# Kernel optimization log

Hardware: AMD Instinct MI355X
Metric: run time of the kernel (lower is better)

The kernel has to match this reference:

```python
import jax, jax.numpy as jnp
import numpy as np

FC = 16  # feat_channel
EPS = 1e-4


def _sch_forward(sch_feat, conv_weight, mask, target, pre_ind, ind):
    B, C, H, W = sch_feat.shape
    M = pre_ind.shape[1]
    fc = FC
    # _tranpose_and_gather_feat: gather per-object weight vectors at pre_ind
    cw = conv_weight.reshape(B, conv_weight.shape[1], H * W)          # B,Wt,HW
    weight = jnp.take_along_axis(cw, pre_ind[:, None, :], axis=2)    # B,Wt,M
    weight = jnp.transpose(weight, (0, 2, 1))                         # B,M,Wt
    # split into the 3-layer dynamic MLP params
    s1 = (fc + 2) * fc
    w1 = weight[..., :s1].reshape(B, M, fc, fc + 2)
    b1 = weight[..., s1:s1 + fc]
    s2 = s1 + fc
    w2 = weight[..., s2:s2 + fc * fc].reshape(B, M, fc, fc)
    b2 = weight[..., s2 + fc * fc:s2 + fc * fc + fc]
    s3 = s2 + fc * fc + fc
    w3 = weight[..., s3:s3 + fc]                                      # B,M,fc (1 out channel)
    b3 = weight[..., s3 + fc:s3 + fc + 1]                             # B,M,1
    # relative coordinate grids; note torch: x = pre_ind % w (int), y = pre_ind / w (true div)
    x = (pre_ind % W).astype(jnp.float32)
    y = pre_ind.astype(jnp.float32) / W
    xg = jnp.arange(W, dtype=jnp.float32)
    yg = jnp.arange(H, dtype=jnp.float32)
    x_rel = (xg[None, None, None, :] - x[:, :, None, None]) / 128.0   # B,M,1,W
    y_rel = (yg[None, None, :, None] - y[:, :, None, None]) / 128.0   # B,M,H,1
    x_rel = jnp.broadcast_to(x_rel, (B, M, H, W))
    y_rel = jnp.broadcast_to(y_rel, (B, M, H, W))
    feat = jnp.concatenate([
        jnp.broadcast_to(sch_feat[:, None], (B, M, C, H, W)),
        x_rel[:, :, None], y_rel[:, :, None]], axis=2)                # B,M,fc+2,H,W
    # three grouped 1x1 convs == per-instance matmuls
    h = jax.nn.relu(jnp.einsum('bmchw,bmoc->bmohw', feat, w1) + b1[:, :, :, None, None])
    h = jax.nn.relu(jnp.einsum('bmchw,bmoc->bmohw', h, w2) + b2[:, :, :, None, None])
    hm = jnp.einsum('bmchw,bmc->bmhw', h, w3) + b3[:, :, :, None]      # B,M,H,W
    hm = jnp.clip(jax.nn.sigmoid(hm), EPS, 1.0 - EPS)                  # _sigmoid
    # FastFocalLoss over (B*M, 1, H, W) with cat = 0
    neg_loss = jnp.sum(jnp.log(1.0 - hm) * hm ** 2 * (1.0 - target) ** 4)
    hm_flat = hm.reshape(B, M, H * W)
    pos_pred = jnp.take_along_axis(hm_flat, ind[..., None], axis=2)[..., 0]  # B,M
    pos_loss = jnp.sum(jnp.log(pos_pred) * (1.0 - pos_pred) ** 2 * mask)
    num_pos = jnp.sum(mask)
    loss = jnp.where(num_pos == 0,
                     -neg_loss,
                     -(pos_loss + neg_loss) / jnp.maximum(num_pos, 1.0))
    return loss


def setup_inputs() -> dict:
    key = jax.random.key(0)
    k1, k2, k3, k4, k5 = jax.random.split(key, 5)
    B, M, H, W = 4, 32, 152, 272
    Wt = (FC + 2) * FC + FC + FC * FC + FC + FC + 1  # 593
    return {
        'sch_feat': jax.random.normal(k1, (B, FC, H, W), dtype=jnp.float32),
        'conv_weight': jax.random.normal(k2, (B, Wt, H, W), dtype=jnp.float32),
        'mask': jnp.ones((B, M), dtype=jnp.float32),
        'pre_ind': jax.random.randint(k3, (B, M), 0, H * W, dtype=jnp.int64) if jax.config.jax_enable_x64 else jax.random.randint(k3, (B, M), 0, H * W).astype(jnp.int32),
        'target': jax.random.uniform(k4, (B, M, H, W), dtype=jnp.float32),
        'ind': jax.random.randint(k5, (B, M), 0, H * W).astype(jnp.int32),
    }


def reference(sch_feat, conv_weight, mask, pre_ind, target, ind):
    return _sch_forward(sch_feat, conv_weight, mask, target, pre_ind, ind)
```

## Files before the change

### kernel.cpp

```cpp
#include <hip/hip_runtime.h>

typedef unsigned int uint;
typedef unsigned short ushort;

constexpr int Bc = 4, Mc = 32, Hc = 152, Wc = 272;
constexpr int HWc = Hc * Wc;
constexpr int WTc = 593;
constexpr int MG = 4;
constexpr int MPB = 8;
constexpr int NBCH = 64;
constexpr int NEG_BLOCKS = Bc * MG * NBCH;
constexpr int ITERS = HWc / 64;
constexpr int POS_OFF = 1024;
constexpr int APK1_OFF = 2048;
constexpr int APK2_OFF = APK1_OFF + 128 * 64 * 4;
constexpr int W3B3_OFF = APK2_OFF + 128 * 64 * 4;
constexpr int CB_OFF   = W3B3_OFF + 128 * 20;
constexpr size_t XOFF_BYTES = (size_t)(CB_OFF + 128 * 32) * 4;
constexpr int GRPB = HWc / 16;
constexpr int GSTRIDE = 576;
constexpr int XCVT_BLOCKS = 162 * Bc;

using f32x4 = __attribute__((ext_vector_type(4))) float;
using bf16x8 = __attribute__((ext_vector_type(8))) short;

__device__ inline uint pkbf(float lo, float hi) {
  uint r;
  asm("v_cvt_pk_bf16_f32 %0, %1, %2" : "=v"(r) : "v"(lo), "v"(hi));
  return r;
}

__device__ inline float xsum16(float x) {
#if __has_builtin(__builtin_amdgcn_permlane16_swap)
  uint u = __float_as_uint(x);
  auto pr = __builtin_amdgcn_permlane16_swap(u, u, false, false);
  return __uint_as_float(pr[0]) + __uint_as_float(pr[1]);
#else
  return x + __shfl_xor(x, 16);
#endif
}
__device__ inline float xsum32(float x) {
#if __has_builtin(__builtin_amdgcn_permlane32_swap)
  uint u = __float_as_uint(x);
  auto pr = __builtin_amdgcn_permlane32_swap(u, u, false, false);
  return __uint_as_float(pr[0]) + __uint_as_float(pr[1]);
#else
  return x + __shfl_xor(x, 32);
#endif
}

union FR { uint u[4]; bf16x8 v; };

__global__ __launch_bounds__(256) void fused_pre(const float* __restrict__ sf_all,
                                                 const float* __restrict__ cw,
                                                 const int* __restrict__ pre_ind,
                                                 const int* __restrict__ ind,
                                                 const float* __restrict__ mask,
                                                 unsigned char* __restrict__ xb,
                                                 float* __restrict__ ws) {
  __shared__ float sw[WTc];
  __shared__ float sh1[16], sh2[16];
  const int blk = blockIdx.x, tid = threadIdx.x;

  if (blk < XCVT_BLOCKS) {
    const int b = blk / 162, bx = blk - b * 162;
    const int px = bx * 256 + tid;
    if (px < HWc) {
      const float* s = sf_all + (size_t)b * 16 * HWc + px;
      uint q[8];
#pragma unroll
      for (int i = 0; i < 8; i++) q[i] = pkbf(s[(size_t)(2 * i) * HWc], s[(size_t)(2 * i + 1) * HWc]);
      const int hh = px / Wc, xx = px - hh * Wc;
      const uint q8 = pkbf((float)xx * 0.0078125f, (float)hh * 0.0078125f);
      const int grp = px >> 4, o = px & 15;
      unsigned char* gb = xb + ((size_t)b * GRPB + grp) * GSTRIDE;
      *(uint4*)(gb + o * 16) = make_uint4(q[0], q[1], q[2], q[3]);
      *(uint4*)(gb + 256 + o * 16) = make_uint4(q[4], q[5], q[6], q[7]);
      *(uint*)(gb + 512 + o * 4) = q8;
    }
    return;
  }

  const int bm = blk - XCVT_BLOCKS, b = bm >> 5;
  const int p = pre_ind[bm];
  const float* wcol = cw + (size_t)b * WTc * HWc + p;
  for (int j = tid; j < WTc; j += 256) sw[j] = wcol[(size_t)j * HWc];
  __syncthreads();

  const float x0 = (float)(p % Wc);
  const float y0 = (float)p / (float)Wc;

  if (tid < 64) {
    const int g = tid >> 4, o = tid & 15;
    float a1f[8], a2f[8];
#pragma unroll
    for (int e = 0; e < 8; e++) {
      int k = 8 * g + e;
      a1f[e] = (k < 18) ? sw[o * 18 + k] : 0.0f;
      a2f[e] = (e < 4) ? sw[304 + o * 16 + 4 * g + e] : 0.0f;
    }
    uint4 u1, u2;
    u1.x = pkbf(a1f[0], a1f[1]); u1.y = pkbf(a1f[2], a1f[3]);
    u1.z = pkbf(a1f[4], a1f[5]); u1.w = pkbf(a1f[6], a1f[7]);
    u2.x = pkbf(a2f[0], a2f[1]); u2.y = pkbf(a2f[2], a2f[3]);
    u2.z = 0u; u2.w = 0u;
    ((uint4*)(ws + APK1_OFF))[bm * 64 + tid] = u1;
    ((uint4*)(ws + APK2_OFF))[bm * 64 + tid] = u2;
  } else if (tid >= 80 && tid < 97) {
    const int k = tid - 80;
    ws[W3B3_OFF + bm * 20 + k] = (k < 16) ? sw[576 + k] : sw[592];
  } else if (tid >= 100 && tid < 116) {
    const int row = tid - 100;
    ws[CB_OFF + bm * 32 + row] =
        sw[288 + row] - (sw[row * 18 + 16] * x0 + sw[row * 18 + 17] * y0) * 0.0078125f;
    ws[CB_OFF + bm * 32 + 16 + row] = sw[560 + row];
  }

  if (tid >= 64 && tid < 80) {
    const int oo = tid - 64;
    const float* sf = sf_all + (size_t)b * 16 * HWc;
    const int pi = ind[bm];
    float f[18];
#pragma unroll
    for (int c = 0; c < 16; c++) f[c] = sf[(size_t)c * HWc + pi];
    const int hh = pi / Wc;
    f[16] = ((float)(pi - hh * Wc) - x0) * 0.0078125f;
    f[17] = ((float)hh - y0) * 0.0078125f;
    float a = sw[288 + oo];
#pragma unroll
    for (int c = 0; c < 18; c++) a = fmaf(sw[oo * 18 + c], f[c], a);
    sh1[oo] = fmaxf(a, 0.0f);
  }
  __syncthreads();
  if (tid >= 64 && tid < 80) {
    const int oo = tid - 64;
    float a = sw[560 + oo];
#pragma unroll
    for (int c = 0; c < 16; c++) a = fmaf(sw[304 + oo * 16 + c], sh1[c], a);
    sh2[oo] = fmaxf(a, 0.0f);
  }
  __syncthreads();
  if (tid == 64) {
    float zv = sw[592];
#pragma unroll
    for (int c = 0; c < 16; c++) zv = fmaf(sw[576 + c], sh2[c], zv);
    float hm = __fdividef(1.0f, 1.0f + __expf(-zv));
    hm = fminf(fmaxf(hm, 1e-4f), 1.0f - 1e-4f);
    const float om = 1.0f - hm;
    ws[POS_OFF + bm] = __logf(hm) * om * om * mask[bm];
  }
}

__global__ __launch_bounds__(256, 4) void sch_neg(const float* __restrict__ target,
                                                  const unsigned char* __restrict__ xbf,
                                                  float* __restrict__ ws) {
  __shared__ uint4 sA1[MPB][64];
  __shared__ uint2 sA2[MPB][64];
  __shared__ float sW3[MPB][20];
  __shared__ float sCB[MPB][32];
  __shared__ float red[256];

  const int tid = threadIdx.x;
  const int lane = tid & 63;
  const int wid = tid >> 6;
  const int xcd = blockIdx.x & 7;
  const int slot = blockIdx.x >> 3;
  const int b = xcd >> 1;
  const int mg = slot & 3;
  const int nb = ((slot >> 2) << 1) | (xcd & 1);
  const int bmBase = b * 32 + mg * MPB;

  for (int e = tid; e < MPB * 64; e += 256) {
    const int j = e >> 6, l = e & 63;
    sA1[j][l] = ((const uint4*)(ws + APK1_OFF))[(bmBase + j) * 64 + l];
    uint4 a2 = ((const uint4*)(ws + APK2_OFF))[(bmBase + j) * 64 + l];
    sA2[j][l] = make_uint2(a2.x, a2.y);
  }
  for (int e = tid; e < MPB * 20; e += 256)
    sW3[e / 20][e % 20] = ws[W3B3_OFF + (bmBase + e / 20) * 20 + (e % 20)];
  for (int e = tid; e < MPB * 32; e += 256)
    sCB[e >> 5][e & 31] = ws[CB_OFF + (bmBase + (e >> 5)) * 32 + (e & 31)];
  __syncthreads();

  const int g = lane >> 4, o = lane & 15;
  const unsigned char* xb = xbf + (size_t)b * GRPB * GSTRIDE;
  const float* tg0 = target + (size_t)bmBase * HWc;
  const int addrOff = (g < 2) ? ((g << 8) + (o << 4)) : (512 + (o << 2));
  const int wslot = nb * 4 + wid;
  const int itS = (wslot * ITERS) >> 8;
  const int itE = ((wslot + 1) * ITERS) >> 8;

  float acc = 0.0f;
  for (int it = itS; it < itE; ++it) {
    const unsigned char* gb = xb + (size_t)it * (4 * GSTRIDE);
    uint4 ld[4];
#pragma unroll
    for (int c = 0; c < 4; c++) ld[c] = *(const uint4*)(gb + c * GSTRIDE + addrOff);
    const int off64 = it * 64 + lane;

#pragma unroll 1
    for (int j = 0; j < MPB; ++j) {
      FR A1, A2;
      {
        uint4 u1 = sA1[j][lane];
        A1.u[0] = u1.x; A1.u[1] = u1.y; A1.u[2] = u1.z; A1.u[3] = u1.w;
        uint2 u2 = sA2[j][lane];
        A2.u[0] = u2.x; A2.u[1] = u2.y; A2.u[2] = 0u; A2.u[3] = 0u;
      }
      const f32x4 cw3 = *(const f32x4*)&sW3[j][g * 4];
      const float b3v = sW3[j][16];
      const f32x4 cc1 = *(const f32x4*)&sCB[j][g * 4];
      const f32x4 cc2 = *(const f32x4*)&sCB[j][16 + g * 4];
      const float tval = tg0[(size_t)j * HWc + off64];

      float Z[4];
#pragma unroll
      for (int c = 0; c < 4; c++) {
        FR B1;
        B1.u[0] = ld[c].x; B1.u[1] = ld[c].y; B1.u[2] = ld[c].z; B1.u[3] = ld[c].w;
        f32x4 d1 = __builtin_amdgcn_mfma_f32_16x16x32_bf16(A1.v, B1.v, cc1, 0, 0, 0);
        FR B2;
        B2.u[0] = pkbf(fmaxf(d1[0], 0.0f), fmaxf(d1[1], 0.0f));
        B2.u[1] = pkbf(fmaxf(d1[2], 0.0f), fmaxf(d1[3], 0.0f));
        B2.u[2] = 0u; B2.u[3] = 0u;
        f32x4 d2 = __builtin_amdgcn_mfma_f32_16x16x32_bf16(A2.v, B2.v, cc2, 0, 0, 0);
        float zp = fmaxf(d2[0], 0.0f) * cw3[0] + fmaxf(d2[1], 0.0f) * cw3[1] +
                   fmaxf(d2[2], 0.0f) * cw3[2] + fmaxf(d2[3], 0.0f) * cw3[3];
        Z[c] = xsum32(xsum16(zp));
      }
      float zz = (lane & 32) ? ((lane & 16) ? Z[3] : Z[2]) : ((lane & 16) ? Z[1] : Z[0]);
      zz += b3v;
      float hm = __fdividef(1.0f, 1.0f + __expf(-zz));
      hm = fminf(fmaxf(hm, 1e-4f), 1.0f - 1e-4f);
      const float u = 1.0f - tval;
      const float u2 = u * u;
      acc += __logf(1.0f - hm) * hm * hm * (u2 * u2);
    }
  }

  red[tid] = acc;
  __syncthreads();
  for (int s = 128; s > 0; s >>= 1) {
    if (tid < s) red[tid] += red[tid + s];
    __syncthreads();
  }
  if (tid == 0) ws[blockIdx.x] = red[0];
}

__global__ __launch_bounds__(256) void sch_final(const float* __restrict__ ws,
                                                 const float* __restrict__ mask,
                                                 float* __restrict__ out) {
  __shared__ float red[256];
  const int t = threadIdx.x;

  float s = 0.0f;
  for (int i = t; i < NEG_BLOCKS; i += 256) s += ws[i];
  red[t] = s; __syncthreads();
  for (int k = 128; k > 0; k >>= 1) { if (t < k) red[t] += red[t + k]; __syncthreads(); }
  const float neg = red[0];
  __syncthreads();

  float pv = (t < Bc * Mc) ? ws[POS_OFF + t] : 0.0f;
  red[t] = pv; __syncthreads();
  for (int k = 128; k > 0; k >>= 1) { if (t < k) red[t] += red[t + k]; __syncthreads(); }
  const float pos = red[0];
  __syncthreads();

  float mv = (t < Bc * Mc) ? mask[t] : 0.0f;
  red[t] = mv; __syncthreads();
  for (int k = 128; k > 0; k >>= 1) { if (t < k) red[t] += red[t + k]; __syncthreads(); }

  if (t == 0) {
    float np = red[0];
    out[0] = (np == 0.0f) ? (-neg) : (-(pos + neg) / fmaxf(np, 1.0f));
  }
}

extern "C" void kernel_launch(void* const* d_in, const int* in_sizes, int n_in,
                              void* d_out, int out_size, void* d_ws, size_t ws_size,
                              hipStream_t stream) {
  const float* sch_feat    = (const float*)d_in[0];
  const float* conv_weight = (const float*)d_in[1];
  const float* mask        = (const float*)d_in[2];
  const int*   pre_ind     = (const int*)d_in[3];
  const float* target      = (const float*)d_in[4];
  const int*   ind         = (const int*)d_in[5];
  float* out = (float*)d_out;
  float* ws  = (float*)d_ws;
  unsigned char* xbf = (unsigned char*)d_ws + XOFF_BYTES;

  fused_pre<<<dim3(XCVT_BLOCKS + Bc * Mc), dim3(256), 0, stream>>>(
      sch_feat, conv_weight, pre_ind, ind, mask, xbf, ws);
  sch_neg<<<dim3(NEG_BLOCKS), dim3(256), 0, stream>>>(target, xbf, ws);
  sch_final<<<dim3(1), dim3(256), 0, stream>>>(ws, mask, out);
}
```

Measured before the change: 50.25 us.

## Fuse preprocessing into main loss kernel, recomputing weights and bf16 features per block

Removes the separate preprocessing kernel. Each main-kernel block now gathers its 8 objects' dynamic weights from conv_weight into shared memory, packs the MFMA operands itself, and computes the positive loss term in a single designated block per group. The per-pixel bf16 feature packing now happens inline: each wave reads fp32 features, converts them, and stages them in a per-wave LDS tile instead of reading a precomputed global buffer. This saves a launch and the global round trip of the packed buffer. In exchange, every block gathers the weights redundantly (strided, uncoalesced reads) and the feature conversion is repeated across the four object groups.

```diff
diff --git a/kernel.cpp b/kernel.cpp
--- a/kernel.cpp
+++ b/kernel.cpp
@@ -1,25 +1,15 @@
 #include <hip/hip_runtime.h>
 
 typedef unsigned int uint;
-typedef unsigned short ushort;
 
 constexpr int Bc = 4, Mc = 32, Hc = 152, Wc = 272;
 constexpr int HWc = Hc * Wc;
 constexpr int WTc = 593;
 constexpr int MG = 4;
 constexpr int MPB = 8;
-constexpr int NBCH = 64;
-constexpr int NEG_BLOCKS = Bc * MG * NBCH;
+constexpr int NEG_BLOCKS = 1024;
 constexpr int ITERS = HWc / 64;
 constexpr int POS_OFF = 1024;
-constexpr int APK1_OFF = 2048;
-constexpr int APK2_OFF = APK1_OFF + 128 * 64 * 4;
-constexpr int W3B3_OFF = APK2_OFF + 128 * 64 * 4;
-constexpr int CB_OFF   = W3B3_OFF + 128 * 20;
-constexpr size_t XOFF_BYTES = (size_t)(CB_OFF + 128 * 32) * 4;
-constexpr int GRPB = HWc / 16;
-constexpr int GSTRIDE = 576;
-constexpr int XCVT_BLOCKS = 162 * Bc;
 
 using f32x4 = __attribute__((ext_vector_type(4))) float;
 using bf16x8 = __attribute__((ext_vector_type(8))) short;
@@ -29,7 +19,6 @@
   asm("v_cvt_pk_bf16_f32 %0, %1, %2" : "=v"(r) : "v"(lo), "v"(hi));
   return r;
 }
-
 __device__ inline float xsum16(float x) {
 #if __has_builtin(__builtin_amdgcn_permlane16_swap)
   uint u = __float_as_uint(x);
@@ -51,113 +40,20 @@
 
 union FR { uint u[4]; bf16x8 v; };
 
-__global__ __launch_bounds__(256) void fused_pre(const float* __restrict__ sf_all,
-                                                 const float* __restrict__ cw,
-                                                 const int* __restrict__ pre_ind,
-                                                 const int* __restrict__ ind,
-                                                 const float* __restrict__ mask,
-                                                 unsigned char* __restrict__ xb,
-                                                 float* __restrict__ ws) {
-  __shared__ float sw[WTc];
-  __shared__ float sh1[16], sh2[16];
-  const int blk = blockIdx.x, tid = threadIdx.x;
-
-  if (blk < XCVT_BLOCKS) {
-    const int b = blk / 162, bx = blk - b * 162;
-    const int px = bx * 256 + tid;
-    if (px < HWc) {
-      const float* s = sf_all + (size_t)b * 16 * HWc + px;
-      uint q[8];
-#pragma unroll
-      for (int i = 0; i < 8; i++) q[i] = pkbf(s[(size_t)(2 * i) * HWc], s[(size_t)(2 * i + 1) * HWc]);
-      const int hh = px / Wc, xx = px - hh * Wc;
-      const uint q8 = pkbf((float)xx * 0.0078125f, (float)hh * 0.0078125f);
-      const int grp = px >> 4, o = px & 15;
-      unsigned char* gb = xb + ((size_t)b * GRPB + grp) * GSTRIDE;
-      *(uint4*)(gb + o * 16) = make_uint4(q[0], q[1], q[2], q[3]);
-      *(uint4*)(gb + 256 + o * 16) = make_uint4(q[4], q[5], q[6], q[7]);
-      *(uint*)(gb + 512 + o * 4) = q8;
-    }
-    return;
-  }
-
-  const int bm = blk - XCVT_BLOCKS, b = bm >> 5;
-  const int p = pre_ind[bm];
-  const float* wcol = cw + (size_t)b * WTc * HWc + p;
-  for (int j = tid; j < WTc; j += 256) sw[j] = wcol[(size_t)j * HWc];
-  __syncthreads();
-
-  const float x0 = (float)(p % Wc);
-  const float y0 = (float)p / (float)Wc;
-
-  if (tid < 64) {
-    const int g = tid >> 4, o = tid & 15;
-    float a1f[8], a2f[8];
-#pragma unroll
-    for (int e = 0; e < 8; e++) {
-      int k = 8 * g + e;
-      a1f[e] = (k < 18) ? sw[o * 18 + k] : 0.0f;
-      a2f[e] = (e < 4) ? sw[304 + o * 16 + 4 * g + e] : 0.0f;
-    }
-    uint4 u1, u2;
-    u1.x = pkbf(a1f[0], a1f[1]); u1.y = pkbf(a1f[2], a1f[3]);
-    u1.z = pkbf(a1f[4], a1f[5]); u1.w = pkbf(a1f[6], a1f[7]);
-    u2.x = pkbf(a2f[0], a2f[1]); u2.y = pkbf(a2f[2], a2f[3]);
-    u2.z = 0u; u2.w = 0u;
-    ((uint4*)(ws + APK1_OFF))[bm * 64 + tid] = u1;
-    ((uint4*)(ws + APK2_OFF))[bm * 64 + tid] = u2;
-  } else if (tid >= 80 && tid < 97) {
-    const int k = tid - 80;
-    ws[W3B3_OFF + bm * 20 + k] = (k < 16) ? sw[576 + k] : sw[592];
-  } else if (tid >= 100 && tid < 116) {
-    const int row = tid - 100;
-    ws[CB_OFF + bm * 32 + row] =
-        sw[288 + row] - (sw[row * 18 + 16] * x0 + sw[row * 18 + 17] * y0) * 0.0078125f;
-    ws[CB_OFF + bm * 32 + 16 + row] = sw[560 + row];
-  }
-
-  if (tid >= 64 && tid < 80) {
-    const int oo = tid - 64;
-    const float* sf = sf_all + (size_t)b * 16 * HWc;
-    const int pi = ind[bm];
-    float f[18];
-#pragma unroll
-    for (int c = 0; c < 16; c++) f[c] = sf[(size_t)c * HWc + pi];
-    const int hh = pi / Wc;
-    f[16] = ((float)(pi - hh * Wc) - x0) * 0.0078125f;
-    f[17] = ((float)hh - y0) * 0.0078125f;
-    float a = sw[288 + oo];
-#pragma unroll
-    for (int c = 0; c < 18; c++) a = fmaf(sw[oo * 18 + c], f[c], a);
-    sh1[oo] = fmaxf(a, 0.0f);
-  }
-  __syncthreads();
-  if (tid >= 64 && tid < 80) {
-    const int oo = tid - 64;
-    float a = sw[560 + oo];
-#pragma unroll
-    for (int c = 0; c < 16; c++) a = fmaf(sw[304 + oo * 16 + c], sh1[c], a);
-    sh2[oo] = fmaxf(a, 0.0f);
-  }
-  __syncthreads();
-  if (tid == 64) {
-    float zv = sw[592];
-#pragma unroll
-    for (int c = 0; c < 16; c++) zv = fmaf(sw[576 + c], sh2[c], zv);
-    float hm = __fdividef(1.0f, 1.0f + __expf(-zv));
-    hm = fminf(fmaxf(hm, 1e-4f), 1.0f - 1e-4f);
-    const float om = 1.0f - hm;
-    ws[POS_OFF + bm] = __logf(hm) * om * om * mask[bm];
-  }
-}
-
-__global__ __launch_bounds__(256, 4) void sch_neg(const float* __restrict__ target,
-                                                  const unsigned char* __restrict__ xbf,
-                                                  float* __restrict__ ws) {
+__global__ __launch_bounds__(256, 4) void sch_fused(const float* __restrict__ sf_all,
+                                                    const float* __restrict__ cw,
+                                                    const int* __restrict__ pre_ind,
+                                                    const int* __restrict__ ind,
+                                                    const float* __restrict__ mask,
+                                                    const float* __restrict__ target,
+                                                    float* __restrict__ ws) {
+  __shared__ float stage[4][600];
   __shared__ uint4 sA1[MPB][64];
   __shared__ uint2 sA2[MPB][64];
   __shared__ float sW3[MPB][20];
   __shared__ float sCB[MPB][32];
+  __shared__ float sh1[4][16], sh2[4][16];
+  __shared__ uint  xp[4][768];
   __shared__ float red[256];
 
   const int tid = threadIdx.x;
@@ -169,34 +65,119 @@
   const int mg = slot & 3;
   const int nb = ((slot >> 2) << 1) | (xcd & 1);
   const int bmBase = b * 32 + mg * MPB;
-
-  for (int e = tid; e < MPB * 64; e += 256) {
-    const int j = e >> 6, l = e & 63;
-    sA1[j][l] = ((const uint4*)(ws + APK1_OFF))[(bmBase + j) * 64 + l];
-    uint4 a2 = ((const uint4*)(ws + APK2_OFF))[(bmBase + j) * 64 + l];
-    sA2[j][l] = make_uint2(a2.x, a2.y);
-  }
-  for (int e = tid; e < MPB * 20; e += 256)
-    sW3[e / 20][e % 20] = ws[W3B3_OFF + (bmBase + e / 20) * 20 + (e % 20)];
-  for (int e = tid; e < MPB * 32; e += 256)
-    sCB[e >> 5][e & 31] = ws[CB_OFF + (bmBase + (e >> 5)) * 32 + (e & 31)];
-  __syncthreads();
-
   const int g = lane >> 4, o = lane & 15;
-  const unsigned char* xb = xbf + (size_t)b * GRPB * GSTRIDE;
+  const bool posBlock = (nb == 0);
+
+  const float* sf = sf_all + (size_t)b * 16 * HWc;
+
+  for (int rnd = 0; rnd < 2; ++rnd) {
+    const int m0 = rnd * 4;
+    for (int e = tid; e < 4 * WTc; e += 256) {
+      const int mj = e / WTc, j = e - mj * WTc;
+      const int p = pre_ind[bmBase + m0 + mj];
+      stage[mj][j] = cw[((size_t)b * WTc + j) * HWc + p];
+    }
+    __syncthreads();
+
+    if (tid < 64) {
+#pragma unroll
+      for (int mj = 0; mj < 4; ++mj) {
+        float a1f[8], a2f[8];
+#pragma unroll
+        for (int e = 0; e < 8; e++) {
+          int k = 8 * g + e;
+          a1f[e] = (k < 18) ? stage[mj][o * 18 + k] : 0.0f;
+          a2f[e] = (e < 4) ? stage[mj][304 + o * 16 + 4 * g + e] : 0.0f;
+        }
+        uint4 u1; uint2 u2;
+        u1.x = pkbf(a1f[0], a1f[1]); u1.y = pkbf(a1f[2], a1f[3]);
+        u1.z = pkbf(a1f[4], a1f[5]); u1.w = pkbf(a1f[6], a1f[7]);
+        u2.x = pkbf(a2f[0], a2f[1]); u2.y = pkbf(a2f[2], a2f[3]);
+        sA1[m0 + mj][tid] = u1;
+        sA2[m0 + mj][tid] = u2;
+      }
+    } else if (tid >= 128 && tid < 192) {
+      const int mj = (tid - 128) >> 4, row = tid & 15;
+      const int p = pre_ind[bmBase + m0 + mj];
+      const float x0 = (float)(p % Wc);
+      const float y0 = (float)p / (float)Wc;
+      sCB[m0 + mj][row] = stage[mj][288 + row] -
+          (stage[mj][row * 18 + 16] * x0 + stage[mj][row * 18 + 17] * y0) * 0.0078125f;
+      sCB[m0 + mj][16 + row] = stage[mj][560 + row];
+    } else if (tid >= 192) {
+      const int mj = (tid - 192) >> 4, k = tid & 15;
+      sW3[m0 + mj][k] = stage[mj][576 + k];
+      if (k == 0) sW3[m0 + mj][16] = stage[mj][592];
+    }
+    if (posBlock && tid >= 64 && tid < 128) {
+      const int mj = (tid - 64) >> 4, row = tid & 15;
+      const int bm = bmBase + m0 + mj;
+      const int p = pre_ind[bm];
+      const int pi = ind[bm];
+      const float x0 = (float)(p % Wc);
+      const float y0 = (float)p / (float)Wc;
+      float f[18];
+#pragma unroll
+      for (int c = 0; c < 16; c++) f[c] = sf[(size_t)c * HWc + pi];
+      const int hh = pi / Wc;
+      f[16] = ((float)(pi - hh * Wc) - x0) * 0.0078125f;
+      f[17] = ((float)hh - y0) * 0.0078125f;
+      float a = stage[mj][288 + row];
+#pragma unroll
+      for (int c = 0; c < 18; c++) a = fmaf(stage[mj][row * 18 + c], f[c], a);
+      sh1[mj][row] = fmaxf(a, 0.0f);
+    }
+    __syncthreads();
+    if (posBlock && tid >= 64 && tid < 128) {
+      const int mj = (tid - 64) >> 4, row = tid & 15;
+      float a = stage[mj][560 + row];
+#pragma unroll
+      for (int c = 0; c < 16; c++) a = fmaf(stage[mj][304 + row * 16 + c], sh1[mj][c], a);
+      sh2[mj][row] = fmaxf(a, 0.0f);
+    }
+    __syncthreads();
+    if (posBlock && tid >= 64 && tid < 128 && (tid & 15) == 0) {
+      const int mj = (tid - 64) >> 4;
+      const int bm = bmBase + m0 + mj;
+      float zv = stage[mj][592];
+#pragma unroll
+      for (int c = 0; c < 16; c++) zv = fmaf(stage[mj][576 + c], sh2[mj][c], zv);
+      float hm = __fdividef(1.0f, 1.0f + __expf(-zv));
+      hm = fminf(fmaxf(hm, 1e-4f), 1.0f - 1e-4f);
+      const float om = 1.0f - hm;
+      ws[POS_OFF + bm] = __logf(hm) * om * om * mask[bm];
+    }
+    __syncthreads();
+  }
+
   const float* tg0 = target + (size_t)bmBase * HWc;
-  const int addrOff = (g < 2) ? ((g << 8) + (o << 4)) : (512 + (o << 2));
+  uint* xpw = xp[wid];
+  const int rdOff = (g < 2) ? (g * 4) : 8;
   const int wslot = nb * 4 + wid;
   const int itS = (wslot * ITERS) >> 8;
   const int itE = ((wslot + 1) * ITERS) >> 8;
 
   float acc = 0.0f;
   for (int it = itS; it < itE; ++it) {
-    const unsigned char* gb = xb + (size_t)it * (4 * GSTRIDE);
+    const int base = it * 64, px = base + lane;
+    const float* s = sf + px;
+    float cv[16];
+#pragma unroll
+    for (int c = 0; c < 16; c++) cv[c] = s[(size_t)c * HWc];
+    uint pk[8];
+#pragma unroll
+    for (int q = 0; q < 8; q++) pk[q] = pkbf(cv[2 * q], cv[2 * q + 1]);
+    const int hh = px / Wc, xx = px - hh * Wc;
+    const uint qc = pkbf((float)xx * 0.0078125f, (float)hh * 0.0078125f);
+    uint* row = xpw + lane * 12;
+    *(uint4*)(row + 0) = make_uint4(pk[0], pk[1], pk[2], pk[3]);
+    *(uint4*)(row + 4) = make_uint4(pk[4], pk[5], pk[6], pk[7]);
+    *(uint4*)(row + 8) = make_uint4(qc, 0u, 0u, 0u);
+    asm volatile("s_waitcnt lgkmcnt(0)" ::: "memory");
+    __builtin_amdgcn_sched_barrier(0);
     uint4 ld[4];
 #pragma unroll
-    for (int c = 0; c < 4; c++) ld[c] = *(const uint4*)(gb + c * GSTRIDE + addrOff);
-    const int off64 = it * 64 + lane;
+    for (int c = 0; c < 4; c++) ld[c] = *(const uint4*)(xpw + (16 * c + o) * 12 + rdOff);
 
 #pragma unroll 1
     for (int j = 0; j < MPB; ++j) {
@@ -211,7 +192,7 @@
       const float b3v = sW3[j][16];
       const f32x4 cc1 = *(const f32x4*)&sCB[j][g * 4];
       const f32x4 cc2 = *(const f32x4*)&sCB[j][16 + g * 4];
-      const float tval = tg0[(size_t)j * HWc + off64];
+      const float tval = tg0[(size_t)j * HWc + base + lane];
 
       float Z[4];
 #pragma unroll
@@ -240,8 +221,8 @@
 
   red[tid] = acc;
   __syncthreads();
-  for (int s = 128; s > 0; s >>= 1) {
-    if (tid < s) red[tid] += red[tid + s];
+  for (int s2 = 128; s2 > 0; s2 >>= 1) {
+    if (tid < s2) red[tid] += red[tid + s2];
     __syncthreads();
   }
   if (tid == 0) ws[blockIdx.x] = red[0];
@@ -287,10 +268,8 @@
   const int*   ind         = (const int*)d_in[5];
   float* out = (float*)d_out;
   float* ws  = (float*)d_ws;
-  unsigned char* xbf = (unsigned char*)d_ws + XOFF_BYTES;
-
-  fused_pre<<<dim3(XCVT_BLOCKS + Bc * Mc), dim3(256), 0, stream>>>(
-      sch_feat, conv_weight, pre_ind, ind, mask, xbf, ws);
-  sch_neg<<<dim3(NEG_BLOCKS), dim3(256), 0, stream>>>(target, xbf, ws);
+
+  sch_fused<<<dim3(NEG_BLOCKS), dim3(256), 0, stream>>>(
+      sch_feat, conv_weight, pre_ind, ind, mask, target, ws);
   sch_final<<<dim3(1), dim3(256), 0, stream>>>(ws, mask, out);
 }
```

Result: slower. 60.94 us (+21.3%).
